# Kernel tuning notes

Measured on AMD Instinct MI355X. Metric: run time of the kernel, lower is better.

The kernel has to match this reference:

```python
import jax, jax.numpy as jnp
import numpy as np

PATCH = 8
EPS = 1e-5

def patch_split(x, s):
    # B C H W -> B s*s rH rW C
    B, C, H, W = x.shape
    rH, rW = H // s, W // s
    out = x.reshape(B, C, s, rH, s, rW)
    out = out.transpose(0, 2, 4, 3, 5, 1)
    return out.reshape(B, s * s, rH, rW, C)

def patch_recover(x, s):
    # B s*s rH rW C -> B C H W
    B, N, rH, rW, C = x.shape
    out = x.reshape(B, s, s, rH, rW, C)
    out = out.transpose(0, 5, 1, 3, 2, 4)
    return out.reshape(B, C, s * rH, s * rW)

def conv2d(x, w, pad):
    return jax.lax.conv_general_dilated(x, w, (1, 1), [(pad, pad), (pad, pad)],
                                        dimension_numbers=('NCHW', 'OIHW', 'NCHW'))

def bn_relu(x, g, b):
    # eval-mode BatchNorm2d with fresh running stats (mean=0, var=1)
    scale = (g / jnp.sqrt(1.0 + EPS))[None, :, None, None]
    return jax.nn.relu(x * scale + b[None, :, None, None])


def setup_inputs() -> dict:
    key = jax.random.key(0)
    ks = jax.random.split(key, 24)
    r = lambda i, shape, s=0.02: jax.random.normal(ks[i], shape, jnp.float32) * s
    B, H, W, C, K, P = 4, 64, 64, 512, 19, 64
    return {
        'M_1': jax.random.normal(ks[0], (B, 2048, H, W), jnp.float32),
        'F': jax.random.normal(ks[1], (B, C, H, W), jnp.float32),
        'I': jax.random.normal(ks[2], (B, K, H, W), jnp.float32),
        'R': jax.random.uniform(ks[3], (B, K, PATCH, PATCH), jnp.float32),
        'lg_w1': r(4, (P, P)), 'lg_w2': r(5, (C, C)),
        'fuse_w': r(6, (P,)), 'fuse_b': r(7, (1,)),
        'q_w': r(8, (256, C)), 'q_b': r(9, (256,)),
        'k_w': r(10, (256, C)), 'k_b': r(11, (256,)),
        'v_w': r(12, (256, C)), 'v_b': r(13, (256,)),
        'c1_w': r(14, (512, 256, 1, 1)),
        'bn1_g': jnp.ones((512,)), 'bn1_b': jnp.zeros((512,)),
        'c2_w': r(15, (512, 512, 3, 3)),
        'bn2_g': jnp.ones((512,)), 'bn2_b': jnp.zeros((512,)),
        'c3_w': r(16, (512, 2560, 3, 3)),
        'bn3_g': jnp.ones((512,)), 'bn3_b': jnp.zeros((512,)),
        'drop_w': r(17, (K, 512, 1, 1)),
    }


def reference(M_1, F, I, R, lg_w1, lg_w2, fuse_w, fuse_b, q_w, q_b, k_w, k_b,
              v_w, v_b, c1_w, bn1_g, bn1_b, c2_w, bn2_g, bn2_b, c3_w, bn3_g,
              bn3_b, drop_w):
    B = F.shape[0]
    F_p5 = patch_split(F, PATCH)          # B P rH rW C
    _, P, rH, rW, C = F_p5.shape
    I_p5 = patch_split(I, PATCH)          # B P rH rW K
    K = I_p5.shape[-1]
    F_p = F_p5.reshape(B, P, rH * rW, C)
    I_p = I_p5.reshape(B, P, rH * rW, K)
    bin_conf = R.reshape(B, K, P).transpose(0, 2, 1)[..., None]  # B P K 1
    pix = jax.nn.softmax(I_p, axis=2)
    F_l = jnp.einsum('bpnk,bpnc->bpkc', pix, F_p) * bin_conf     # B P K C
    # LG block: 1x1 conv over P channels, residual relu, linear over C
    h = jnp.einsum('qp,bpkc->bqkc', lg_w1, F_l)
    h = jax.nn.relu(h + F_l)
    F_l = jnp.einsum('bpkc,dc->bpkd', h, lg_w2)
    # FUSE: 1x1 conv P->1 (with bias); broadcast replaces torch .repeat
    F_g = jnp.einsum('p,bpkc->bkc', fuse_w, F_l) + fuse_b        # B K C
    query = jnp.einsum('bpnc,dc->bpnd', F_p, q_w) + q_b          # B P N 256
    key_ = jnp.einsum('bpkc,dc->bpkd', F_l, k_w) + k_b           # B P K 256
    value = jnp.einsum('bkc,dc->bkd', F_g, v_w) + v_b            # B K 256
    aff = jax.nn.softmax(jnp.einsum('bpnd,bpkd->bpnk', query, key_), axis=-1)
    F_s = jnp.einsum('bpnk,bkd->bpnd', aff, value)               # B P N 256
    F_s = patch_recover(F_s.reshape(B, P, rH, rW, -1), PATCH)    # B 256 H W
    Fo1 = F + bn_relu(conv2d(F_s, c1_w, 0), bn1_g, bn1_b)
    x2 = bn_relu(conv2d(Fo1, c2_w, 1), bn2_g, bn2_b)
    x3 = bn_relu(conv2d(jnp.concatenate([x2, M_1], axis=1), c3_w, 1), bn3_g, bn3_b)
    # Dropout2d is identity in eval; final 1x1 classifier conv
    return conv2d(x3, drop_w, 0)
```

## Files before the change

### kernel.cpp

```cpp
#include <hip/hip_runtime.h>
#include <hip/hip_bf16.h>

typedef __hip_bfloat16 bf16;
using short8 = __attribute__((ext_vector_type(8))) short;
using f32x4  = __attribute__((ext_vector_type(4))) float;

__device__ __forceinline__ float b2f(bf16 v){ return __bfloat162float(v); }
__device__ __forceinline__ bf16  f2b(float v){ return __float2bfloat16(v); }

#define EPSV 1e-5f

__device__ __forceinline__ void gload16(const void* g, void* l) {
  __builtin_amdgcn_global_load_lds(
      (const __attribute__((address_space(1))) unsigned int*)g,
      (__attribute__((address_space(3))) unsigned int*)l, 16, 0, 0);
}

__global__ __launch_bounds__(256) void k_cast(const float* __restrict__ in,
                                              bf16* __restrict__ out, int n4) {
  int i = blockIdx.x * 256 + threadIdx.x;
  if (i < n4) {
    float4 v = ((const float4*)in)[i];
    union { ushort4 u; bf16 h[4]; } o;
    o.h[0] = f2b(v.x); o.h[1] = f2b(v.y); o.h[2] = f2b(v.z); o.h[3] = f2b(v.w);
    ((ushort4*)out)[i] = o.u;
  }
}

__global__ __launch_bounds__(256) void k_wtr(const float* __restrict__ w,
                                             bf16* __restrict__ wt, int CI) {
  int oc = blockIdx.x, c0 = blockIdx.y * 128;
  __shared__ float ld[128 * 9];
  const float* src = w + ((size_t)oc * CI + c0) * 9;
  for (int i = threadIdx.x; i < 128 * 9; i += 256) ld[i] = src[i];
  __syncthreads();
  for (int i = threadIdx.x; i < 128 * 9; i += 256) {
    int k9 = i / 128, t = i - k9 * 128;
    wt[((size_t)k9 * 512 + oc) * CI + c0 + t] = f2b(ld[t * 9 + k9]);
  }
}

__global__ __launch_bounds__(256) void k_m1t(const float* __restrict__ M1,
                                             bf16* __restrict__ M1b) {
  int b = blockIdx.x >> 6, y = blockIdx.x & 63;
  int c0 = blockIdx.y * 64;
  __shared__ float t[64][65];
  for (int i = threadIdx.x; i < 4096; i += 256) {
    int cc = i >> 6, x = i & 63;
    t[x][cc] = M1[((size_t)(b * 2048 + c0 + cc) * 64 + y) * 64 + x];
  }
  __syncthreads();
  for (int i = threadIdx.x; i < 4096; i += 256) {
    int x = i >> 6, cc = i & 63;
    M1b[((size_t)((b * 64 + y) * 64 + x)) * 2048 + c0 + cc] = f2b(t[x][cc]);
  }
}

__global__ __launch_bounds__(256) void k_fp2(const float* __restrict__ F,
                                             bf16* __restrict__ FP) {
  int b = blockIdx.x >> 6, y = blockIdx.x & 63;
  int tid = threadIdx.x;
  __shared__ float t[256][65];
  int p_hi = (y >> 3) << 3, n_hi = (y & 7) << 3;
  for (int half = 0; half < 2; half++) {
    int c0 = half << 8;
    for (int i = tid; i < 256 * 64; i += 256) {
      int cc = i >> 6, x = i & 63;
      t[cc][x] = F[((size_t)(b * 512 + c0 + cc) * 64 + y) * 64 + x];
    }
    __syncthreads();
    for (int x = 0; x < 64; x++) {
      int p = p_hi + (x >> 3), n = n_hi + (x & 7);
      FP[((size_t)(b * 64 + p)) * 32768 + n * 512 + c0 + tid] = f2b(t[tid][x]);
    }
    __syncthreads();
  }
}

__global__ __launch_bounds__(256) void k_flocal2(const float* __restrict__ I,
        const float* __restrict__ R, const bf16* __restrict__ FP,
        float* __restrict__ FL0) {
  int bp = blockIdx.x, b = bp >> 6, p = bp & 63;
  int tid = threadIdx.x, w = tid >> 6, lane = tid & 63;
  __shared__ __align__(16) bf16 fps[64 * 512];
  __shared__ float pix[19][64];
  __shared__ float bc[19];
  {
    const bf16* src = FP + (size_t)bp * 32768 + lane * 8;
    #pragma unroll
    for (int t = 0; t < 16; t++) {
      int chunk = w + t * 4;
      gload16(src + chunk * 512, (char*)fps + chunk * 1024);
    }
  }
  int py = (p >> 3) * 8, px = (p & 7) * 8;
  for (int i = tid; i < 19 * 64; i += 256) {
    int k = i >> 6, n = i & 63;
    int y = py + (n >> 3), x = px + (n & 7);
    pix[k][n] = I[((size_t)(b * 19 + k) * 64 + y) * 64 + x];
  }
  if (tid < 19) bc[tid] = R[(size_t)(b * 19 + tid) * 64 + p];
  __syncthreads();
  if (tid < 19) {
    float mx = -1e30f;
    for (int n = 0; n < 64; n++) mx = fmaxf(mx, pix[tid][n]);
    float s = 0.f;
    for (int n = 0; n < 64; n++) { float e = __expf(pix[tid][n] - mx); pix[tid][n] = e; s += e; }
    float sc = bc[tid] / s;
    for (int n = 0; n < 64; n++) pix[tid][n] *= sc;
  }
  __syncthreads();
  for (int task = tid; task < 19 * 64; task += 256) {
    int k = task >> 6, c8 = (task & 63) << 3;
    float acc[8] = {};
    for (int n = 0; n < 64; n++) {
      float pv = pix[k][n];
      union { short8 s; bf16 h[8]; } v;
      v.s = *(const short8*)&fps[n * 512 + c8];
      #pragma unroll
      for (int j = 0; j < 8; j++) acc[j] += pv * b2f(v.h[j]);
    }
    float* dst = FL0 + ((size_t)(b * 64 + p) * 19 + k) * 512 + c8;
    #pragma unroll
    for (int j = 0; j < 8; j++) dst[j] = acc[j];
  }
}

__global__ __launch_bounds__(256) void k_lg1(const float* __restrict__ FL0,
        const float* __restrict__ w1, bf16* __restrict__ Hb) {
  int tid = threadIdx.x;
  int b = blockIdx.y;
  int n0 = blockIdx.x * 256;
  __shared__ float W[64][64];
  __shared__ float Xs[16][256];
  for (int i = tid; i < 4096; i += 256) W[i >> 6][i & 63] = w1[i];
  float acc[64];
  #pragma unroll
  for (int po = 0; po < 64; po++) acc[po] = 0.f;
  for (int q0 = 0; q0 < 64; q0 += 16) {
    __syncthreads();
    for (int i = tid; i < 4096; i += 256) {
      int q = i >> 8, j = i & 255;
      Xs[q][j] = FL0[(size_t)(b * 64 + q0 + q) * 9728 + n0 + j];
    }
    __syncthreads();
    for (int q = 0; q < 16; q++) {
      float xv = Xs[q][tid];
      #pragma unroll
      for (int po = 0; po < 64; po++) acc[po] += W[po][q0 + q] * xv;
    }
  }
  for (int po = 0; po < 64; po++) {
    float r = acc[po] + FL0[(size_t)(b * 64 + po) * 9728 + n0 + tid];
    Hb[(size_t)(b * 64 + po) * 9728 + n0 + tid] = f2b(fmaxf(r, 0.f));
  }
}

template<int MODE>
__global__ __launch_bounds__(256) void k_gmm(
    const bf16* __restrict__ A, const bf16* __restrict__ B,
    const float* __restrict__ bias, float* __restrict__ C,
    bf16* __restrict__ Cb, int N, int K,
    const float* __restrict__ g, const float* __restrict__ bb,
    const float* __restrict__ Fres, bf16* __restrict__ outb) {
  int tid = threadIdx.x;
  int m0 = blockIdx.x * 128, n0 = blockIdx.y * 128;
  int w = tid >> 6, lane = tid & 63, ln = lane & 15, qd = lane >> 4;
  int wm = w & 1, wn = w >> 1;
  __shared__ __align__(16) char smem[34816];

  f32x4 acc[4][4];
  #pragma unroll
  for (int i = 0; i < 4; i++)
    #pragma unroll
    for (int j = 0; j < 4; j++) acc[i][j] = (f32x4){0.f, 0.f, 0.f, 0.f};

  int rsub = lane >> 2, ch = lane & 3;
  auto stage = [&](int p) {
    char* base = smem + (p & 1) * 16384;
    int k0 = p << 5;
    #pragma unroll
    for (int t = 0; t < 2; t++) {
      int ii = w + t * 4;
      int r = ii * 16 + rsub;
      int sw = (ch ^ ((r >> 1) & 3)) << 3;
      gload16(A + (size_t)(m0 + r) * K + k0 + sw, base + ii * 1024);
      gload16(B + (size_t)(n0 + r) * K + k0 + sw, base + 8192 + ii * 1024);
    }
  };
  auto compute = [&](int p) {
    const char* base = smem + (p & 1) * 16384;
    short8 af[4], bv[4];
    #pragma unroll
    for (int mi = 0; mi < 4; mi++) {
      int r = wm * 64 + mi * 16 + ln;
      af[mi] = *(const short8*)(base + r * 64 + ((qd ^ ((r >> 1) & 3)) << 4));
    }
    #pragma unroll
    for (int ni = 0; ni < 4; ni++) {
      int r = wn * 64 + ni * 16 + ln;
      bv[ni] = *(const short8*)(base + 8192 + r * 64 + ((qd ^ ((r >> 1) & 3)) << 4));
    }
    #pragma unroll
    for (int mi = 0; mi < 4; mi++)
      #pragma unroll
      for (int ni = 0; ni < 4; ni++)
        acc[mi][ni] = __builtin_amdgcn_mfma_f32_16x16x32_bf16(
            af[mi], bv[ni], acc[mi][ni], 0, 0, 0);
  };

  int KT = K >> 5;
  stage(0);
  __syncthreads();
  for (int p = 0; p < KT; p++) {
    if (p + 1 < KT) stage(p + 1);
    compute(p);
    __syncthreads();
  }

  if (MODE <= 1) {
    #pragma unroll
    for (int mi = 0; mi < 4; mi++) {
      #pragma unroll
      for (int r = 0; r < 4; r++) {
        int m = m0 + wm * 64 + mi * 16 + qd * 4 + r;
        #pragma unroll
        for (int ni = 0; ni < 4; ni++) {
          int n = n0 + wn * 64 + ni * 16 + ln;
          float v = acc[mi][ni][r];
          if (bias) v += bias[n];
          C[(size_t)m * N + n] = v;
          if (MODE == 1) Cb[(size_t)m * N + n] = f2b(v);
        }
      }
    }
  } else {
    bf16* EP = (bf16*)smem;
    int b = n0 >> 12;
    #pragma unroll
    for (int mi = 0; mi < 4; mi++) {
      #pragma unroll
      for (int r = 0; r < 4; r++) {
        int ml = wm * 64 + mi * 16 + qd * 4 + r;
        int oc = m0 + ml;
        float sc = g[oc] * rsqrtf(1.f + EPSV);
        float bt = bb[oc];
        #pragma unroll
        for (int ni = 0; ni < 4; ni++) {
          int nl = wn * 64 + ni * 16 + ln;
          int pix = n0 + nl;
          int y = (pix >> 6) & 63, x = pix & 63;
          float v = fmaxf(acc[mi][ni][r] * sc + bt, 0.f)
                  + Fres[((size_t)(b * 512 + oc) * 64 + y) * 64 + x];
          EP[nl * 136 + ml] = f2b(v);
        }
      }
    }
    __syncthreads();
    int pl = tid >> 1, half = tid & 1;
    size_t gb = (size_t)(n0 + pl) * 512 + m0 + half * 64;
    const bf16* row = &EP[pl * 136 + half * 64];
    #pragma unroll
    for (int j2 = 0; j2 < 8; j2++)
      *(short8*)(outb + gb + j2 * 8) = *(const short8*)(row + j2 * 8);
  }
}

__global__ __launch_bounds__(256) void k_fusev(const float* __restrict__ FL,
        const float* __restrict__ fw, const float* __restrict__ fbv,
        const float* __restrict__ vw, const float* __restrict__ vb,
        float* __restrict__ VAL) {
  int tid = threadIdx.x;
  int bk = blockIdx.x, b = bk / 19, k = bk % 19;
  __shared__ float fwl[64];
  __shared__ __align__(16) float fg[512];
  if (tid < 64) fwl[tid] = fw[tid];
  __syncthreads();
  float fbias = fbv[0];
  for (int c = tid; c < 512; c += 256) {
    float s = 0.f;
    for (int p = 0; p < 64; p++)
      s += fwl[p] * FL[((size_t)(b * 64 + p) * 19 + k) * 512 + c];
    fg[c] = s + fbias;
  }
  __syncthreads();
  int d = tid;
  float s = vb[d];
  const float4* vr = (const float4*)(vw + (size_t)d * 512);
  const float4* fr = (const float4*)fg;
  for (int c4 = 0; c4 < 128; c4++) {
    float4 wv = vr[c4], f = fr[c4];
    s += f.x * wv.x + f.y * wv.y + f.z * wv.z + f.w * wv.w;
  }
  VAL[(size_t)bk * 256 + d] = s;
}

__global__ __launch_bounds__(256) void k_attn(const float* __restrict__ Q,
        const float* __restrict__ KEY, const float* __restrict__ VAL,
        bf16* __restrict__ FS) {
  int tid = threadIdx.x;
  int bp = blockIdx.x, b = bp >> 6, p = bp & 63;
  __shared__ __align__(16) float ks[19][256];
  __shared__ __align__(16) float vs[19][256];
  __shared__ float Ss[64][20];
  __shared__ bf16 ot[64][256];
  for (int i = tid; i < 19 * 256; i += 256) {
    ks[i >> 8][i & 255] = KEY[(size_t)bp * 19 * 256 + i];
    vs[i >> 8][i & 255] = VAL[(size_t)b * 19 * 256 + i];
  }
  __syncthreads();
  {
    int n = tid >> 2, kq = tid & 3;
    const float4* qrow = (const float4*)(Q + ((size_t)bp * 64 + n) * 256);
    for (int k = kq; k < 19; k += 4) {
      const float4* kr = (const float4*)&ks[k][0];
      float s = 0.f;
      for (int d4 = 0; d4 < 64; d4++) {
        float4 qv = qrow[d4], kv = kr[d4];
        s += qv.x * kv.x + qv.y * kv.y + qv.z * kv.z + qv.w * kv.w;
      }
      Ss[n][k] = s;
    }
  }
  __syncthreads();
  if (tid < 64) {
    float mx = -1e30f;
    for (int k = 0; k < 19; k++) mx = fmaxf(mx, Ss[tid][k]);
    float sum = 0.f;
    for (int k = 0; k < 19; k++) { float e = __expf(Ss[tid][k] - mx); Ss[tid][k] = e; sum += e; }
    float inv = 1.f / sum;
    for (int k = 0; k < 19; k++) Ss[tid][k] *= inv;
  }
  __syncthreads();
  {
    int d = tid;
    for (int nn = 0; nn < 64; nn++) {
      float s = 0.f;
      #pragma unroll
      for (int k = 0; k < 19; k++) s += Ss[nn][k] * vs[k][d];
      ot[nn][d] = f2b(s);
    }
  }
  __syncthreads();
  {
    int py = (p >> 3) * 8, px = (p & 7) * 8;
    int nn = tid >> 2, q = tid & 3;
    int y = py + (nn >> 3), x = px + (nn & 7);
    size_t gb = (((size_t)(b * 64 + y) * 64) + x) * 256 + q * 64;
    const bf16* row = &ot[nn][q * 64];
    #pragma unroll
    for (int j = 0; j < 8; j++)
      *(short8*)(FS + gb + j * 8) = *(const short8*)(row + j * 8);
  }
}

__global__ __launch_bounds__(256) void k_conv3(
    const bf16* __restrict__ Xin, int Cin,
    const bf16* __restrict__ M1b, const float* __restrict__ M1f, int C2,
    const bf16* __restrict__ WT,
    const float* __restrict__ g, const float* __restrict__ bb,
    bf16* __restrict__ out, int Cos) {
  int tid = threadIdx.x;
  int b = blockIdx.x >> 4, y0 = (blockIdx.x & 15) * 4;
  int oc0 = blockIdx.y * 128;
  int w = tid >> 6, lane = tid & 63, ln = lane & 15, qd = lane >> 4;
  int wocg = w & 1, wyp = w >> 1;
  int Ct = Cin + C2;

  __shared__ __align__(16) char smem[49152 + 25344];
  char* smA = smem;
  char* smB = smem + 49152;

  for (int i = tid; i < 6 * 2 * 32; i += 256) {
    int rl = i >> 6, hh = (i >> 5) & 1, kk = i & 31;
    *(bf16*)(smB + (rl * 66 + (hh ? 65 : 0)) * 64 + kk * 2) = f2b(0.f);
  }
  if (y0 == 0)
    for (int i = tid; i < 66 * 16; i += 256) ((float*)smB)[i] = 0.f;
  if (y0 == 60)
    for (int i = tid; i < 66 * 16; i += 256)
      ((float*)(smB + 5 * 66 * 64))[i] = 0.f;

  f32x4 acc[4][8];
  #pragma unroll
  for (int i = 0; i < 4; i++)
    #pragma unroll
    for (int j = 0; j < 8; j++) acc[i][j] = (f32x4){0.f, 0.f, 0.f, 0.f};

  int NPH = (Ct >> 5) * 3;

  auto stageA = [&](int p) {
    int c0 = (p / 3) << 5, ky = p % 3;
    char* base = smA + (p & 1) * 24576;
    int j = w;
    #pragma unroll
    for (int t = 0; t < 6; t++, j += 4) {
      int kx = j >> 3, i8 = j & 7;
      int ocl = i8 * 16 + (lane >> 2);
      const bf16* src = WT + ((size_t)((ky * 3 + kx) * 512 + oc0 + ocl) * Ct + c0)
                      + (((lane & 3) ^ ((ocl >> 1) & 3)) << 3);
      gload16(src, base + (kx * 128 + i8 * 16) * 64);
    }
  };
  auto stageB = [&](int gi) {
    int c0 = gi << 5;
    if (c0 < Cin || M1b != nullptr) {
      const bf16* T; int Cs, cb;
      if (c0 < Cin) { T = Xin; Cs = Cin; cb = c0; }
      else          { T = M1b; Cs = C2;  cb = c0 - Cin; }
      int j = w;
      #pragma unroll
      for (int t = 0; t < 6; t++, j += 4) {
        int rl = j >> 2, i4 = j & 3;
        int yy = y0 + rl - 1;
        if ((unsigned)yy < 64u) {
          int xx = i4 * 16 + (lane >> 2), xr = xx + 1;
          const bf16* src = T + ((size_t)((b * 64 + yy) * 64 + xx) * Cs + cb)
                          + (((lane & 3) ^ ((xr >> 1) & 3)) << 3);
          gload16(src, smB + (rl * 66 + 1 + i4 * 16) * 64);
        }
      }
    } else {
      #pragma unroll
      for (int t = 0; t < 2; t++) {
        int rl = w + t * 4;
        if (rl < 6) {
          int yy = y0 + rl - 1;
          if ((unsigned)yy < 64u) {
            int xx = lane, xr = xx + 1;
            const float* mp = M1f + ((size_t)(b * 2048 + (c0 - Cin)) * 64 + yy) * 64 + xx;
            #pragma unroll
            for (int q = 0; q < 8; q++) {
              union { ushort4 u; bf16 h[4]; } pk;
              #pragma unroll
              for (int jj = 0; jj < 4; jj++) pk.h[jj] = f2b(mp[(size_t)(q * 4 + jj) * 4096]);
              *(ushort4*)(smB + (rl * 66 + xr) * 64
                          + ((((q >> 1) ^ ((xr >> 1) & 3)) << 4) | ((q & 1) << 3))) = pk.u;
            }
          }
        }
      }
    }
  };
  auto computeP = [&](int p) {
    int ky = p % 3;
    const char* base = smA + (p & 1) * 24576;
    int rl0 = 2 * wyp + ky;
    #pragma unroll
    for (int kx = 0; kx < 3; kx++) {
      short8 af[4], bv[8];
      #pragma unroll
      for (int mi = 0; mi < 4; mi++) {
        int ocl = wocg * 64 + mi * 16 + ln;
        af[mi] = *(const short8*)(base + (kx * 128 + ocl) * 64
                                  + ((qd ^ ((ocl >> 1) & 3)) << 4));
      }
      #pragma unroll
      for (int ni = 0; ni < 8; ni++) {
        int rl = rl0 + (ni >> 2);
        int xr = (ni & 3) * 16 + ln + kx;
        bv[ni] = *(const short8*)(smB + (rl * 66 + xr) * 64
                                  + ((qd ^ ((xr >> 1) & 3)) << 4));
      }
      #pragma unroll
      for (int mi = 0; mi < 4; mi++)
        #pragma unroll
        for (int ni = 0; ni < 8; ni++)
          acc[mi][ni] = __builtin_amdgcn_mfma_f32_16x16x32_bf16(
              af[mi], bv[ni], acc[mi][ni], 0, 0, 0);
    }
  };

  stageB(0);
  stageA(0);
  __syncthreads();
  for (int p = 0; p < NPH; p++) {
    if (p + 1 < NPH && (p + 1) % 3 != 0) stageA(p + 1);
    computeP(p);
    __syncthreads();
    if (p + 1 < NPH && (p + 1) % 3 == 0) {
      stageA(p + 1);
      stageB((p + 1) / 3);
      __syncthreads();
    }
  }

  {
    bf16* EP = (bf16*)smem;
    #pragma unroll
    for (int mi = 0; mi < 4; mi++) {
      int oclb = wocg * 64 + mi * 16 + qd * 4;
      float sc[4], bt[4];
      #pragma unroll
      for (int r = 0; r < 4; r++) {
        int oc = oc0 + oclb + r;
        sc[r] = g[oc] * rsqrtf(1.f + EPSV);
        bt[r] = bb[oc];
      }
      #pragma unroll
      for (int ni = 0; ni < 8; ni++) {
        int yloc = 2 * wyp + (ni >> 2), x = (ni & 3) * 16 + ln;
        union { ushort4 u; bf16 h[4]; } pk;
        #pragma unroll
        for (int r = 0; r < 4; r++)
          pk.h[r] = f2b(fmaxf(acc[mi][ni][r] * sc[r] + bt[r], 0.f));
        *(ushort4*)&EP[(yloc * 64 + x) * 128 + oclb] = pk.u;
      }
    }
    __syncthreads();
    int p2 = tid >> 1, hh = tid & 1;
    #pragma unroll
    for (int pp = 0; pp < 2; pp++) {
      int pixl = pp * 128 + p2;
      int yloc = pixl >> 6, x = pixl & 63;
      size_t gb = ((size_t)((b * 64 + y0 + yloc) * 64 + x)) * Cos + oc0 + hh * 64;
      const bf16* row = &EP[pixl * 128 + hh * 64];
      #pragma unroll
      for (int k = 0; k < 8; k++)
        *(short8*)(out + gb + k * 8) = *(const short8*)(row + k * 8);
    }
  }
}

__global__ __launch_bounds__(256) void k_final(const bf16* __restrict__ X3,
        const float* __restrict__ dw, float* __restrict__ out) {
  int tid = threadIdx.x;
  int b = blockIdx.x >> 6, y = blockIdx.x & 63;
  __shared__ float W[19 * 512];
  for (int i = tid; i < 19 * 512; i += 256) W[i] = dw[i];
  __syncthreads();
  int x = tid & 63, kg = tid >> 6;
  const bf16* px = X3 + (((size_t)(b * 64 + y) * 64) + x) * 512;
  float acc[5] = {0.f, 0.f, 0.f, 0.f, 0.f};
  for (int c8 = 0; c8 < 512; c8 += 8) {
    union { short8 s; bf16 h[8]; } v;
    v.s = *(const short8*)(px + c8);
    float f[8];
    #pragma unroll
    for (int j = 0; j < 8; j++) f[j] = b2f(v.h[j]);
    #pragma unroll
    for (int i = 0; i < 5; i++) {
      int k = kg * 5 + i;
      if (k < 19) {
        const float* wr = &W[k * 512 + c8];
        #pragma unroll
        for (int j = 0; j < 8; j++) acc[i] += f[j] * wr[j];
      }
    }
  }
  for (int i = 0; i < 5; i++) {
    int k = kg * 5 + i;
    if (k < 19) out[((size_t)(b * 19 + k) * 64 + y) * 64 + x] = acc[i];
  }
}

extern "C" void kernel_launch(void* const* d_in, const int* in_sizes, int n_in,
                              void* d_out, int out_size, void* d_ws, size_t ws_size,
                              hipStream_t stream) {
  (void)in_sizes; (void)n_in; (void)out_size;
  const float* M1 = (const float*)d_in[0];
  const float* F  = (const float*)d_in[1];
  const float* Iin= (const float*)d_in[2];
  const float* R  = (const float*)d_in[3];
  const float* w1 = (const float*)d_in[4];
  const float* w2 = (const float*)d_in[5];
  const float* fw = (const float*)d_in[6];
  const float* fb = (const float*)d_in[7];
  const float* qw = (const float*)d_in[8];
  const float* qb = (const float*)d_in[9];
  const float* kw = (const float*)d_in[10];
  const float* kb = (const float*)d_in[11];
  const float* vw = (const float*)d_in[12];
  const float* vb = (const float*)d_in[13];
  const float* c1 = (const float*)d_in[14];
  const float* g1 = (const float*)d_in[15];
  const float* b1 = (const float*)d_in[16];
  const float* c2 = (const float*)d_in[17];
  const float* g2 = (const float*)d_in[18];
  const float* b2 = (const float*)d_in[19];
  const float* c3 = (const float*)d_in[20];
  const float* g3 = (const float*)d_in[21];
  const float* b3 = (const float*)d_in[22];
  const float* dw = (const float*)d_in[23];

  char* ws = (char*)d_ws;
  bool fast = ws_size >= (size_t)137363456ULL;

  bf16*  qwb  = (bf16*)(ws + 0);
  bf16*  kwb  = (bf16*)(ws + 262144);
  bf16*  w2b  = (bf16*)(ws + 524288);
  bf16*  c1b  = (bf16*)(ws + 1048576);
  bf16*  WT2  = (bf16*)(ws + 0);
  bf16*  WT3  = (bf16*)(ws + 4718592);
  bf16*  FS   = (bf16*)(ws + 28311552);
  bf16*  FO1  = (bf16*)(ws + 36700160);
  bf16*  X2   = (bf16*)(ws + 53477376);
  bf16*  M1bf = fast ? (bf16*)(ws + 70254592) : nullptr;
  bf16*  X3   = (bf16*)(ws + 28311552);
  bf16*  FP    = (bf16*) (ws + 53477376);
  float* QUERY = (float*)(ws + 70254592);
  float* FL0   = (float*)(ws + 87031808);
  bf16*  Hb    = (bf16*) (ws + 96993280);
  bf16*  FLb   = (bf16*) (ws + 101974016);
  float* KEY   = (float*)(ws + 106954752);
  float* VAL   = (float*)(ws + 111935488);
  float* FL    = FL0;

  k_cast<<<128, 256, 0, stream>>>(qw, qwb, 32768);
  k_cast<<<128, 256, 0, stream>>>(kw, kwb, 32768);
  k_cast<<<256, 256, 0, stream>>>(w2, w2b, 65536);
  k_cast<<<128, 256, 0, stream>>>(c1, c1b, 32768);
  k_fp2<<<256, 256, 0, stream>>>(F, FP);
  k_flocal2<<<256, 256, 0, stream>>>(Iin, R, FP, FL0);
  k_lg1<<<dim3(38, 4), 256, 0, stream>>>(FL0, w1, Hb);
  k_gmm<1><<<dim3(38, 4), 256, 0, stream>>>(Hb, w2b, nullptr, FL, FLb, 512, 512,
                                            nullptr, nullptr, nullptr, nullptr);
  k_fusev<<<76, 256, 0, stream>>>(FL, fw, fb, vw, vb, VAL);
  k_gmm<0><<<dim3(38, 2), 256, 0, stream>>>(FLb, kwb, kb, KEY, nullptr, 256, 512,
                                            nullptr, nullptr, nullptr, nullptr);
  k_gmm<0><<<dim3(128, 2), 256, 0, stream>>>(FP, qwb, qb, QUERY, nullptr, 256, 512,
                                             nullptr, nullptr, nullptr, nullptr);
  k_attn<<<256, 256, 0, stream>>>(QUERY, KEY, VAL, FS);
  if (fast) k_m1t<<<dim3(256, 32), 256, 0, stream>>>(M1, M1bf);
  k_gmm<2><<<dim3(4, 128), 256, 0, stream>>>(c1b, FS, nullptr, nullptr, nullptr,
                                             16384, 256, g1, b1, F, FO1);
  k_wtr<<<dim3(512, 4),  256, 0, stream>>>(c2, WT2, 512);
  k_wtr<<<dim3(512, 20), 256, 0, stream>>>(c3, WT3, 2560);
  k_conv3<<<dim3(64, 4), 256, 0, stream>>>(FO1, 512, nullptr, nullptr, 0,
                                           WT2, g2, b2, X2, 512);
  k_conv3<<<dim3(64, 4), 256, 0, stream>>>(X2, 512, M1bf, M1, 2048,
                                           WT3, g3, b3, X3, 512);
  k_final<<<256, 256, 0, stream>>>(X3, dw, (float*)d_out);
}
```

Measured before the change: 1.048 ms.

## Double-buffer conv3 input tile and overlap its loads with MFMA compute

Adds a second shared-memory buffer for the input (B) tile so the next channel group's activations load while the current group computes, removing the extra stall and barrier at every third phase. Synchronisation now uses explicit vmcnt waits that count outstanding async LDS loads, plus raw s_barrier. Out-of-range halo rows are sent to a dump region so every lane issues the same number of loads, keeping those counts exact. LDS use rises to about 104KB per block, which may cut occupancy, and the hand-counted waits are fragile.

```diff
diff --git a/kernel.cpp b/kernel.cpp
--- a/kernel.cpp
+++ b/kernel.cpp
@@ -367,19 +367,23 @@
   int wocg = w & 1, wyp = w >> 1;
   int Ct = Cin + C2;
 
-  __shared__ __align__(16) char smem[49152 + 25344];
-  char* smA = smem;
-  char* smB = smem + 49152;
-
-  for (int i = tid; i < 6 * 2 * 32; i += 256) {
-    int rl = i >> 6, hh = (i >> 5) & 1, kk = i & 31;
-    *(bf16*)(smB + (rl * 66 + (hh ? 65 : 0)) * 64 + kk * 2) = f2b(0.f);
-  }
-  if (y0 == 0)
-    for (int i = tid; i < 66 * 16; i += 256) ((float*)smB)[i] = 0.f;
-  if (y0 == 60)
-    for (int i = tid; i < 66 * 16; i += 256)
-      ((float*)(smB + 5 * 66 * 64))[i] = 0.f;
+  __shared__ __align__(16) char smem[103936];
+  char* smA  = smem;
+  char* smB  = smem + 49152;
+  char* dump = smem + 99840;
+
+  for (int bufi = 0; bufi < 2; bufi++) {
+    char* bbuf = smB + bufi * 25344;
+    for (int i = tid; i < 6 * 2 * 32; i += 256) {
+      int rl = i >> 6, hh = (i >> 5) & 1, kk = i & 31;
+      *(bf16*)(bbuf + (rl * 66 + (hh ? 65 : 0)) * 64 + kk * 2) = f2b(0.f);
+    }
+    if (y0 == 0)
+      for (int i = tid; i < 66 * 16; i += 256) ((float*)bbuf)[i] = 0.f;
+    if (y0 == 60)
+      for (int i = tid; i < 66 * 16; i += 256)
+        ((float*)(bbuf + 5 * 66 * 64))[i] = 0.f;
+  }
 
   f32x4 acc[4][8];
   #pragma unroll
@@ -404,21 +408,21 @@
   };
   auto stageB = [&](int gi) {
     int c0 = gi << 5;
+    char* bbuf = smB + (gi & 1) * 25344;
     if (c0 < Cin || M1b != nullptr) {
       const bf16* T; int Cs, cb;
       if (c0 < Cin) { T = Xin; Cs = Cin; cb = c0; }
       else          { T = M1b; Cs = C2;  cb = c0 - Cin; }
-      int j = w;
-      #pragma unroll
-      for (int t = 0; t < 6; t++, j += 4) {
-        int rl = j >> 2, i4 = j & 3;
+      #pragma unroll
+      for (int rl = 0; rl < 6; rl++) {
         int yy = y0 + rl - 1;
-        if ((unsigned)yy < 64u) {
-          int xx = i4 * 16 + (lane >> 2), xr = xx + 1;
-          const bf16* src = T + ((size_t)((b * 64 + yy) * 64 + xx) * Cs + cb)
-                          + (((lane & 3) ^ ((xr >> 1) & 3)) << 3);
-          gload16(src, smB + (rl * 66 + 1 + i4 * 16) * 64);
-        }
+        bool ok = (unsigned)yy < 64u;
+        int yc = ok ? yy : y0;
+        int xx = w * 16 + (lane >> 2), xr = xx + 1;
+        const bf16* src = T + ((size_t)((b * 64 + yc) * 64 + xx) * Cs + cb)
+                        + (((lane & 3) ^ ((xr >> 1) & 3)) << 3);
+        char* dst = ok ? (bbuf + (rl * 66 + 1 + w * 16) * 64) : (dump + w * 1024);
+        gload16(src, dst);
       }
     } else {
       #pragma unroll
@@ -434,7 +438,7 @@
               union { ushort4 u; bf16 h[4]; } pk;
               #pragma unroll
               for (int jj = 0; jj < 4; jj++) pk.h[jj] = f2b(mp[(size_t)(q * 4 + jj) * 4096]);
-              *(ushort4*)(smB + (rl * 66 + xr) * 64
+              *(ushort4*)(bbuf + (rl * 66 + xr) * 64
                           + ((((q >> 1) ^ ((xr >> 1) & 3)) << 4) | ((q & 1) << 3))) = pk.u;
             }
           }
@@ -445,6 +449,7 @@
   auto computeP = [&](int p) {
     int ky = p % 3;
     const char* base = smA + (p & 1) * 24576;
+    const char* bB   = smB + ((p / 3) & 1) * 25344;
     int rl0 = 2 * wyp + ky;
     #pragma unroll
     for (int kx = 0; kx < 3; kx++) {
@@ -459,7 +464,7 @@
       for (int ni = 0; ni < 8; ni++) {
         int rl = rl0 + (ni >> 2);
         int xr = (ni & 3) * 16 + ln + kx;
-        bv[ni] = *(const short8*)(smB + (rl * 66 + xr) * 64
+        bv[ni] = *(const short8*)(bB + (rl * 66 + xr) * 64
                                   + ((qd ^ ((xr >> 1) & 3)) << 4));
       }
       #pragma unroll
@@ -473,17 +478,32 @@
 
   stageB(0);
   stageA(0);
-  __syncthreads();
+  asm volatile("s_waitcnt vmcnt(0)" ::: "memory");
+  __syncthreads();
+
   for (int p = 0; p < NPH; p++) {
-    if (p + 1 < NPH && (p + 1) % 3 != 0) stageA(p + 1);
+    int pn = p + 1;
+    bool hasA = pn < NPH;
+    bool hasB = hasA && (pn % 3 == 0);
+    bool bfast = false;
+    if (hasA) stageA(pn);
+    if (hasB) {
+      int gi = pn / 3;
+      bfast = ((gi << 5) < Cin) || (M1b != nullptr);
+      stageB(gi);
+    }
+    __builtin_amdgcn_sched_barrier(0);
+    if (!hasA)              asm volatile("s_waitcnt vmcnt(0)"  ::: "memory");
+    else if (hasB && bfast) asm volatile("s_waitcnt vmcnt(12)" ::: "memory");
+    else                    asm volatile("s_waitcnt vmcnt(6)"  ::: "memory");
+    __builtin_amdgcn_s_barrier();
+    __builtin_amdgcn_sched_barrier(0);
     computeP(p);
-    __syncthreads();
-    if (p + 1 < NPH && (p + 1) % 3 == 0) {
-      stageA(p + 1);
-      stageB((p + 1) / 3);
-      __syncthreads();
-    }
-  }
+    __builtin_amdgcn_sched_barrier(0);
+    asm volatile("s_waitcnt lgkmcnt(0)" ::: "memory");
+    __builtin_amdgcn_s_barrier();
+  }
+  __syncthreads();
 
   {
     bf16* EP = (bf16*)smem;
```

Measured after the change: 1.019 ms. 2.8% less time.
